# Optimization experiments

Hardware: AMD Instinct MI355X
Metric: run time of the kernel (lower is better)

Reference implementation:

```python
import jax, jax.numpy as jnp
import numpy as np

HEADS = 8
DIM = 512
DIM_HEAD = DIM // 8          # 64
LANDMARKS = DIM // 2         # 256
PINV_ITERS = 6
KERNEL = 33                  # residual_conv_kernel default
SCALE = DIM_HEAD ** -0.5


def setup_inputs() -> dict:
    key = jax.random.key(0)
    k0, k1, k2, k3 = jax.random.split(key, 4)
    b, n = 2, 8192
    x = jax.random.normal(k0, (b, n, DIM), dtype=jnp.float32)
    inner = HEADS * DIM_HEAD
    w_qkv = jax.random.normal(k1, (DIM, 3 * inner), dtype=jnp.float32) * 0.02
    w_out = jax.random.normal(k2, (inner, DIM), dtype=jnp.float32) * 0.02
    b_out = jnp.zeros((DIM,), dtype=jnp.float32)
    # grouped depthwise-over-heads conv: (out_ch=H, in_ch/groups=1, kH=33, kW=1)
    w_conv = jax.random.normal(k3, (HEADS, 1, KERNEL, 1), dtype=jnp.float32) * 0.02
    return {"x": x, "w_qkv": w_qkv, "w_out": w_out, "b_out": b_out, "w_conv": w_conv}


def _moore_penrose_pinv(x, iters=PINV_ITERS):
    # x: [b, h, m, m]
    abs_x = jnp.abs(x)
    col = abs_x.sum(axis=-1).max()   # global max over col sums (matches torch.max)
    row = abs_x.sum(axis=-2).max()
    z = jnp.swapaxes(x, -1, -2) / (col * row)
    I = jnp.eye(x.shape[-1], dtype=x.dtype)
    for _ in range(iters):
        xz = x @ z
        z = 0.25 * z @ (13.0 * I - xz @ (15.0 * I - xz @ (7.0 * I - xz)))
    return z


def reference(x, w_qkv, w_out, b_out, w_conv):
    b, n, _ = x.shape
    m = LANDMARKS
    l = n // m  # n chosen divisible by m, so no left-padding branch

    qkv = x @ w_qkv                                   # [b, n, 3*inner]
    q, k, v = jnp.split(qkv, 3, axis=-1)
    to_heads = lambda t: t.reshape(b, n, HEADS, DIM_HEAD).transpose(0, 2, 1, 3)
    q = to_heads(q) * SCALE                           # [b, h, n, d]
    k = to_heads(k)
    v = to_heads(v)

    # landmarks: mean over consecutive groups of l tokens -> [b, h, m, d]
    q_l = q.reshape(b, HEADS, m, l, DIM_HEAD).mean(axis=3)
    k_l = k.reshape(b, HEADS, m, l, DIM_HEAD).mean(axis=3)

    sim1 = jnp.einsum('bhid,bhjd->bhij', q, k_l)      # [b, h, n, m]
    sim2 = jnp.einsum('bhid,bhjd->bhij', q_l, k_l)    # [b, h, m, m]
    sim3 = jnp.einsum('bhid,bhjd->bhij', q_l, k)      # [b, h, m, n]

    attn1 = jax.nn.softmax(sim1, axis=-1)
    attn2 = jax.nn.softmax(sim2, axis=-1)
    attn3 = jax.nn.softmax(sim3, axis=-1)

    attn2_inv = _moore_penrose_pinv(attn2)
    out = attn1 @ (attn2_inv @ (attn3 @ v))           # [b, h, n, d]

    # residual depthwise conv over the sequence dim, per head (groups = heads)
    pad = KERNEL // 2
    res = jax.lax.conv_general_dilated(
        v, w_conv, window_strides=(1, 1), padding=((pad, pad), (0, 0)),
        dimension_numbers=('NCHW', 'OIHW', 'NCHW'), feature_group_count=HEADS)
    out = out + res

    out = out.transpose(0, 2, 1, 3).reshape(b, n, HEADS * DIM_HEAD)
    out = out @ w_out + b_out                         # to_out (dropout = eval no-op)
    return x + out                                    # NyAttenLayer residual
```

## Files before the change

### kernel.cpp

```cpp
#include <hip/hip_runtime.h>
#include <hip/hip_bf16.h>

#define BH 16
#define NTOK 8192
#define NHEAD 8
#define DH 64
#define MLM 256
#define QSCALE 0.125f
#define LP 72

typedef unsigned short ushort_t;
using frag_ab = __attribute__((ext_vector_type(8))) short;
using frag_cd = __attribute__((ext_vector_type(4))) float;

__device__ __forceinline__ unsigned short f2bs(float f){
  __hip_bfloat16 h = __float2bfloat16(f);
  return *(unsigned short*)&h;
}
__device__ __forceinline__ float bs2f(unsigned short u){
  union { unsigned int i; float f; } cv; cv.i = ((unsigned int)u) << 16; return cv.f;
}

__device__ __forceinline__ void gl_lds16(const unsigned short* g, unsigned short* l){
  __builtin_amdgcn_global_load_lds((const __attribute__((address_space(1))) unsigned int*)(const void*)g,
                                   (__attribute__((address_space(3))) unsigned int*)(void*)l, 16, 0, 0);
}

__global__ __launch_bounds__(256) void k_splitw(const float* __restrict__ in, int K, int N,
                                                unsigned short* __restrict__ oh,
                                                unsigned short* __restrict__ ol, int swz){
  const int idx = blockIdx.x * 256 + threadIdx.x;
  const int n = idx / K, k = idx - n * K;
  const float v = in[(size_t)k * N + n];
  const unsigned short hi = f2bs(v);
  int kd = k;
  if (swz){
    const int q = (k >> 3) & 3;
    kd = (k & ~31) | (((q ^ (n & 3)) & 3) << 3) | (k & 7);
  }
  oh[(size_t)n * K + kd] = hi;
  ol[(size_t)n * K + kd] = f2bs(v - bs2f(hi));
}

__global__ __launch_bounds__(256) void k_splitx(const float* __restrict__ in,
                                                unsigned short* __restrict__ oh,
                                                unsigned short* __restrict__ ol){
  const size_t i4 = ((size_t)blockIdx.x * 256 + threadIdx.x) * 4;
  const int row = (int)(i4 >> 9);
  const int col = (int)(i4 & 511);
  const int q = (col >> 3) & 3;
  const int cd = (col & ~31) | (((q ^ (row & 3)) & 3) << 3) | (col & 7);
  const size_t o4 = ((size_t)row << 9) + cd;
  float4 v = *(const float4*)(in + i4);
  const unsigned short h0 = f2bs(v.x), h1 = f2bs(v.y), h2 = f2bs(v.z), h3 = f2bs(v.w);
  *(ushort4*)(oh + o4) = make_ushort4(h0, h1, h2, h3);
  *(ushort4*)(ol + o4) = make_ushort4(f2bs(v.x - bs2f(h0)), f2bs(v.y - bs2f(h1)),
                                      f2bs(v.z - bs2f(h2)), f2bs(v.w - bs2f(h3)));
}

__global__ __launch_bounds__(256) void k_mfma_qkv(const unsigned short* __restrict__ xh,
                                                  const unsigned short* __restrict__ xl,
                                                  const unsigned short* __restrict__ bth,
                                                  const unsigned short* __restrict__ btl,
                                                  float* __restrict__ q,
                                                  unsigned short* __restrict__ kSh,
                                                  unsigned short* __restrict__ kSl,
                                                  float* __restrict__ v){
  const int n0 = blockIdx.x * 128;
  const int m0 = blockIdx.y * 128;
  __shared__ unsigned short Ah[128*32], Al[128*32], Bh[128*32], Bl[128*32];
  const int tid = threadIdx.x;
  const int wave = tid >> 6, lane = tid & 63;
  const int wm = wave >> 1, wn = wave & 1;
  const int lr = lane & 15, quad = lane >> 4;
  const int cswz = ((quad ^ (lr & 3)) & 3) << 3;
  const unsigned short* gsrc = (wave == 0) ? xh : (wave == 1) ? xl : (wave == 2) ? bth : btl;
  unsigned short* lbase = (wave == 0) ? Ah : (wave == 1) ? Al : (wave == 2) ? Bh : Bl;
  const int R0 = (wave < 2) ? m0 : n0;
  const int lrow = lane >> 2, lslot = (lane & 3) << 3;
  frag_cd acc[4][4];
#pragma unroll
  for (int mt = 0; mt < 4; mt++)
#pragma unroll
    for (int nt = 0; nt < 4; nt++){
      frag_cd z = {0.f, 0.f, 0.f, 0.f};
      acc[mt][nt] = z;
    }
  for (int k0 = 0; k0 < 512; k0 += 32){
    __syncthreads();
#pragma unroll
    for (int u = 0; u < 8; u++){
      gl_lds16(gsrc + (size_t)(R0 + u*16 + lrow) * 512 + k0 + lslot, lbase + u * 512);
    }
    __syncthreads();
    frag_ab a_h[4], a_l[4], b_h[4], b_l[4];
#pragma unroll
    for (int t = 0; t < 4; t++){
      const int ar = (wm*64 + t*16 + lr) << 5;
      const int br = (wn*64 + t*16 + lr) << 5;
      a_h[t] = *(const frag_ab*)&Ah[ar + cswz];
      a_l[t] = *(const frag_ab*)&Al[ar + cswz];
      b_h[t] = *(const frag_ab*)&Bh[br + cswz];
      b_l[t] = *(const frag_ab*)&Bl[br + cswz];
    }
#pragma unroll
    for (int mt = 0; mt < 4; mt++)
#pragma unroll
      for (int nt = 0; nt < 4; nt++){
        acc[mt][nt] = __builtin_amdgcn_mfma_f32_16x16x32_bf16(a_l[mt], b_h[nt], acc[mt][nt], 0, 0, 0);
        acc[mt][nt] = __builtin_amdgcn_mfma_f32_16x16x32_bf16(a_h[mt], b_l[nt], acc[mt][nt], 0, 0, 0);
        acc[mt][nt] = __builtin_amdgcn_mfma_f32_16x16x32_bf16(a_h[mt], b_h[nt], acc[mt][nt], 0, 0, 0);
      }
  }
#pragma unroll
  for (int mt = 0; mt < 4; mt++)
#pragma unroll
    for (int nt = 0; nt < 4; nt++)
#pragma unroll
      for (int rg = 0; rg < 4; rg++){
        const int row = m0 + wm*64 + mt*16 + quad*4 + rg;
        const int col = n0 + wn*64 + nt*16 + lr;
        const int bb = row >> 13, i = row & 8191;
        const int which = col >> 9;
        const int cc = col & 511;
        const int h = cc >> 6, d = cc & 63;
        const size_t off = (((size_t)(bb * NHEAD + h)) * NTOK + i) * DH + d;
        const float val = acc[mt][nt][rg];
        if (which == 0)      q[off] = val * QSCALE;
        else if (which == 1){
          const unsigned short hi = f2bs(val);
          kSh[off] = hi; kSl[off] = f2bs(val - bs2f(hi));
        }
        else                 v[off] = val;
      }
}

__global__ __launch_bounds__(256) void k_mfma_final(const unsigned int* __restrict__ qpk,
                                                    const unsigned short* __restrict__ bth,
                                                    const unsigned short* __restrict__ btl,
                                                    const float* __restrict__ xin,
                                                    const float* __restrict__ bout,
                                                    float* __restrict__ outp){
  const int n0 = blockIdx.x * 128;
  const int m0 = blockIdx.y * 128;
  __shared__ unsigned short Ah[128][40], Al[128][40], Bh[128][40], Bl[128][40];
  const int tid = threadIdx.x;
  const int wave = tid >> 6, lane = tid & 63;
  const int wm = wave >> 1, wn = wave & 1;
  const int lr = lane & 15, quad = lane >> 4, koff = quad * 8;
  const int bb = m0 >> 13;
  frag_cd acc[4][4];
#pragma unroll
  for (int mt = 0; mt < 4; mt++)
#pragma unroll
    for (int nt = 0; nt < 4; nt++){
      frag_cd z = {0.f, 0.f, 0.f, 0.f};
      acc[mt][nt] = z;
    }
  for (int k0 = 0; k0 < 512; k0 += 32){
    const int h = k0 >> 6, dbase = k0 & 63;
    __syncthreads();
#pragma unroll
    for (int u = 0; u < 4; u++){
      const int f = tid + u * 256, row = f >> 3, c4 = (f & 7) << 2;
      const int i = (m0 + row) & 8191;
      uint4 pw = *(const uint4*)(qpk + (((size_t)(bb * NHEAD + h)) * NTOK + i) * DH + dbase + c4);
      *(ushort4*)&Ah[row][c4] = make_ushort4((unsigned short)pw.x, (unsigned short)pw.y,
                                             (unsigned short)pw.z, (unsigned short)pw.w);
      *(ushort4*)&Al[row][c4] = make_ushort4((unsigned short)(pw.x >> 16), (unsigned short)(pw.y >> 16),
                                             (unsigned short)(pw.z >> 16), (unsigned short)(pw.w >> 16));
    }
#pragma unroll
    for (int u = 0; u < 2; u++){
      const int f = tid + u * 256, row = f >> 2, ch = (f & 3) << 3;
      *(uint4*)&Bh[row][ch] = *(const uint4*)(bth + (size_t)(n0 + row) * 512 + k0 + ch);
      *(uint4*)&Bl[row][ch] = *(const uint4*)(btl + (size_t)(n0 + row) * 512 + k0 + ch);
    }
    __syncthreads();
    frag_ab a_h[4], a_l[4], b_h[4], b_l[4];
#pragma unroll
    for (int t = 0; t < 4; t++){
      a_h[t] = *(const frag_ab*)&Ah[wm*64 + t*16 + lr][koff];
      a_l[t] = *(const frag_ab*)&Al[wm*64 + t*16 + lr][koff];
      b_h[t] = *(const frag_ab*)&Bh[wn*64 + t*16 + lr][koff];
      b_l[t] = *(const frag_ab*)&Bl[wn*64 + t*16 + lr][koff];
    }
#pragma unroll
    for (int mt = 0; mt < 4; mt++)
#pragma unroll
      for (int nt = 0; nt < 4; nt++){
        acc[mt][nt] = __builtin_amdgcn_mfma_f32_16x16x32_bf16(a_l[mt], b_h[nt], acc[mt][nt], 0, 0, 0);
        acc[mt][nt] = __builtin_amdgcn_mfma_f32_16x16x32_bf16(a_h[mt], b_l[nt], acc[mt][nt], 0, 0, 0);
        acc[mt][nt] = __builtin_amdgcn_mfma_f32_16x16x32_bf16(a_h[mt], b_h[nt], acc[mt][nt], 0, 0, 0);
      }
  }
#pragma unroll
  for (int mt = 0; mt < 4; mt++)
#pragma unroll
    for (int nt = 0; nt < 4; nt++)
#pragma unroll
      for (int rg = 0; rg < 4; rg++){
        const int row = m0 + wm*64 + mt*16 + quad*4 + rg;
        const int col = n0 + wn*64 + nt*16 + lr;
        outp[(size_t)row * 512 + col] = acc[mt][nt][rg] + bout[col] + xin[(size_t)row * 512 + col];
      }
}

__global__ __launch_bounds__(64) void k_land2(const float* __restrict__ qf,
                                              const unsigned short* __restrict__ kSh,
                                              const unsigned short* __restrict__ kSl,
                                              float* __restrict__ qlf, float* __restrict__ klf,
                                              unsigned short* __restrict__ qlSh, unsigned short* __restrict__ qlSl,
                                              unsigned short* __restrict__ klSh, unsigned short* __restrict__ klSl){
  const int isK = blockIdx.y;
  float* dst = isK ? klf : qlf;
  unsigned short* dh = isK ? klSh : qlSh;
  unsigned short* dl = isK ? klSl : qlSl;
  const int bh = blockIdx.x >> 8;
  const int j  = blockIdx.x & 255;
  const int d  = threadIdx.x;
  const size_t base = ((size_t)bh * NTOK + (size_t)j * 32) * DH + d;
  float s = 0.f;
  if (!isK){
    const float* p = qf + base;
#pragma unroll
    for (int t = 0; t < 32; t++) s += p[t * DH];
  } else {
    const unsigned short* ph = kSh + base;
    const unsigned short* pl = kSl + base;
#pragma unroll
    for (int t = 0; t < 32; t++) s += bs2f(ph[t * DH]) + bs2f(pl[t * DH]);
  }
  const float val = s * (1.f / 32.f);
  const size_t oidx = ((size_t)bh * MLM + j) * DH + d;
  dst[oidx] = val;
  const unsigned short hi = f2bs(val);
  dh[oidx] = hi;
  dl[oidx] = f2bs(val - bs2f(hi));
}

__global__ __launch_bounds__(256) void k_vtrans(const float* __restrict__ vf,
                                                unsigned short* __restrict__ vTh,
                                                unsigned short* __restrict__ vTl){
  __shared__ float T[64][68];
  const int j0 = blockIdx.x * 64, bh = blockIdx.y;
  const int tid = threadIdx.x;
#pragma unroll
  for (int u = 0; u < 4; u++){
    const int f = tid + u * 256, row = f >> 4, c4 = (f & 15) << 2;
    *(float4*)&T[row][c4] = *(const float4*)(vf + ((size_t)bh * NTOK + j0 + row) * DH + c4);
  }
  __syncthreads();
#pragma unroll
  for (int u = 0; u < 4; u++){
    const int f = tid + u * 256, d = f >> 4, j4 = (f & 15) << 2;
    const float v0 = T[j4+0][d], v1 = T[j4+1][d], v2 = T[j4+2][d], v3 = T[j4+3][d];
    const unsigned short h0 = f2bs(v0), h1 = f2bs(v1), h2 = f2bs(v2), h3 = f2bs(v3);
    const size_t off = ((size_t)bh * DH + d) * NTOK + j0 + j4;
    *(ushort4*)(vTh + off) = make_ushort4(h0, h1, h2, h3);
    *(ushort4*)(vTl + off) = make_ushort4(f2bs(v0 - bs2f(h0)), f2bs(v1 - bs2f(h1)),
                                          f2bs(v2 - bs2f(h2)), f2bs(v3 - bs2f(h3)));
  }
}

__global__ __launch_bounds__(256) void k_sim2(const float* __restrict__ qlf,
                                              const float* __restrict__ klf,
                                              float* __restrict__ C){
  const int bh = blockIdx.z;
  const float* Ab = qlf + (size_t)bh * MLM * DH;
  const float* Bb = klf + (size_t)bh * MLM * DH;
  float* Cb = C + (size_t)bh * MLM * MLM;
  const int n0 = blockIdx.x * 64;
  const int m0 = blockIdx.y * 64;
  __shared__ float As[16][64];
  __shared__ float Bs[16][64];
  const int tid = threadIdx.x, ty = tid >> 4, tx = tid & 15;
  const int lm = tid >> 2, lk = (tid & 3) << 2;
  float acc[4][4] = {};
  for (int k0 = 0; k0 < 64; k0 += 16){
    float4 a4 = *(const float4*)(Ab + (size_t)(m0 + lm) * DH + k0 + lk);
    As[lk+0][lm] = a4.x; As[lk+1][lm] = a4.y; As[lk+2][lm] = a4.z; As[lk+3][lm] = a4.w;
    float4 b4 = *(const float4*)(Bb + (size_t)(n0 + lm) * DH + k0 + lk);
    Bs[lk+0][lm] = b4.x; Bs[lk+1][lm] = b4.y; Bs[lk+2][lm] = b4.z; Bs[lk+3][lm] = b4.w;
    __syncthreads();
#pragma unroll
    for (int kk = 0; kk < 16; kk++){
      float a[4], bv[4];
#pragma unroll
      for (int r = 0; r < 4; r++) a[r] = As[kk][ty*4 + r];
#pragma unroll
      for (int c = 0; c < 4; c++) bv[c] = Bs[kk][tx*4 + c];
#pragma unroll
      for (int r = 0; r < 4; r++)
#pragma unroll
        for (int c = 0; c < 4; c++) acc[r][c] += a[r] * bv[c];
    }
    __syncthreads();
  }
#pragma unroll
  for (int r = 0; r < 4; r++)
#pragma unroll
    for (int c = 0; c < 4; c++)
      Cb[(size_t)(m0 + ty*4 + r) * MLM + n0 + tx*4 + c] = acc[r][c];
}

__global__ __launch_bounds__(256) void k_softmax256(const float* __restrict__ in, float* __restrict__ outp){
  const int row = blockIdx.x;
  const int t = threadIdx.x;
  float v = in[(size_t)row * 256 + t];
  __shared__ float red[256];
  red[t] = v; __syncthreads();
  for (int o = 128; o > 0; o >>= 1){ if (t < o) red[t] = fmaxf(red[t], red[t+o]); __syncthreads(); }
  float mx = red[0]; __syncthreads();
  float e = expf(v - mx);
  red[t] = e; __syncthreads();
  for (int o = 128; o > 0; o >>= 1){ if (t < o) red[t] += red[t+o]; __syncthreads(); }
  outp[(size_t)row * 256 + t] = e / red[0];
}

__global__ __launch_bounds__(256) void k_colrow(const float* __restrict__ a2, float* __restrict__ part){
  const int bh = blockIdx.x;
  const int t = threadIdx.x;
  const float* p = a2 + (size_t)bh * 65536;
  float cs = 0.f;
  for (int i = 0; i < 256; i++) cs += fabsf(p[(size_t)i * 256 + t]);
  __shared__ float r2[256];
  r2[t] = cs; __syncthreads();
  for (int o = 128; o > 0; o >>= 1){
    if (t < o) r2[t] = fmaxf(r2[t], r2[t+o]);
    __syncthreads();
  }
  if (t == 0) part[bh] = r2[0];
}

__global__ __launch_bounds__(256) void k_z0(const float* __restrict__ a2, const float* __restrict__ part,
                                            float* __restrict__ z,
                                            unsigned short* __restrict__ zTh,
                                            unsigned short* __restrict__ zTl){
  const int bh = blockIdx.x >> 8;
  const int i  = blockIdx.x & 255;
  const int j  = threadIdx.x;
  float m2 = 0.f;
#pragma unroll
  for (int t = 0; t < 16; t++) m2 = fmaxf(m2, part[t]);
  const float sc = 1.f / m2;
  const size_t ridx = ((size_t)bh * 256 + j) * 256 + i;
  const float val = a2[ridx] * sc;
  z[((size_t)bh * 256 + i) * 256 + j] = val;
  const unsigned short hi = f2bs(val);
  zTh[ridx] = hi;
  zTl[ridx] = f2bs(val - bs2f(hi));
}

__global__ __launch_bounds__(256) void k_gemm256m(const float* __restrict__ A,
                                                  const unsigned short* __restrict__ BTh,
                                                  const unsigned short* __restrict__ BTl,
                                                  const float* __restrict__ D,
                                                  float* __restrict__ C,
                                                  unsigned short* __restrict__ CTh,
                                                  unsigned short* __restrict__ CTl,
                                                  float c0, float s0, int wC){
  __shared__ unsigned short Ah[32][40], Al[32][40], Bh[64][40], Bl[64][40];
  __shared__ float Ct[64][33];
  const int bh = blockIdx.y, tile = blockIdx.x;
  const int m0 = (tile >> 2) * 32, n0 = (tile & 3) * 64;
  const size_t bo = (size_t)bh * 65536;
  const int tid = threadIdx.x;
  const int wave = tid >> 6, lane = tid & 63;
  const int wm = wave >> 1, wn = wave & 1;
  const int lr = lane & 15, quad = lane >> 4, koff = quad * 8;
  const int ar = tid >> 3, ac = (tid & 7) << 2;
  const int br = tid >> 2, bc = (tid & 3) << 3;
  frag_cd acc[2];
  { frag_cd z = {0.f,0.f,0.f,0.f}; acc[0] = z; acc[1] = z; }
  float4 ra  = *(const float4*)(A + bo + (size_t)(m0 + ar) * 256 + ac);
  uint4  rbh = *(const uint4*)(BTh + bo + (size_t)(n0 + br) * 256 + bc);
  uint4  rbl = *(const uint4*)(BTl + bo + (size_t)(n0 + br) * 256 + bc);
  for (int k0 = 0; k0 < 256; k0 += 32){
    __syncthreads();
    {
      const unsigned short h0=f2bs(ra.x),h1=f2bs(ra.y),h2=f2bs(ra.z),h3=f2bs(ra.w);
      *(ushort4*)&Ah[ar][ac] = make_ushort4(h0,h1,h2,h3);
      *(ushort4*)&Al[ar][ac] = make_ushort4(f2bs(ra.x-bs2f(h0)), f2bs(ra.y-bs2f(h1)),
                                            f2bs(ra.z-bs2f(h2)), f2bs(ra.w-bs2f(h3)));
      *(uint4*)&Bh[br][bc] = rbh;
      *(uint4*)&Bl[br][bc] = rbl;
    }
    __syncthreads();
    if (k0 < 224){
      ra  = *(const float4*)(A + bo + (size_t)(m0 + ar) * 256 + k0 + 32 + ac);
      rbh = *(const uint4*)(BTh + bo + (size_t)(n0 + br) * 256 + k0 + 32 + bc);
      rbl = *(const uint4*)(BTl + bo + (size_t)(n0 + br) * 256 + k0 + 32 + bc);
    }
    frag_ab a_h = *(const frag_ab*)&Ah[wm*16 + lr][koff];
    frag_ab a_l = *(const frag_ab*)&Al[wm*16 + lr][koff];
#pragma unroll
    for (int b = 0; b < 2; b++){
      frag_ab b_h = *(const frag_ab*)&Bh[wn*32 + b*16 + lr][koff];
      frag_ab b_l = *(const frag_ab*)&Bl[wn*32 + b*16 + lr][koff];
      acc[b] = __builtin_amdgcn_mfma_f32_16x16x32_bf16(a_l, b_l, acc[b], 0, 0, 0);
      acc[b] = __builtin_amdgcn_mfma_f32_16x16x32_bf16(a_l, b_h, acc[b], 0, 0, 0);
      acc[b] = __builtin_amdgcn_mfma_f32_16x16x32_bf16(a_h, b_l, acc[b], 0, 0, 0);
      acc[b] = __builtin_amdgcn_mfma_f32_16x16x32_bf16(a_h, b_h, acc[b], 0, 0, 0);
    }
  }
  const bool useD = (c0 != 0.f);
#pragma unroll
  for (int b = 0; b < 2; b++)
#pragma unroll
    for (int rg = 0; rg < 4; rg++){
      const int row = m0 + wm*16 + quad*4 + rg;
      const int col = n0 + wn*32 + b*16 + lr;
      const size_t idx = bo + (size_t)row * 256 + col;
      const float dv = useD ? D[idx] : 0.f;
      const float val = s0 * (c0 * dv - acc[b][rg]);
      if (wC) C[idx] = val;
      Ct[col - n0][row - m0] = val;
    }
  __syncthreads();
  {
    const int cr = tid >> 2, sg = (tid & 3) << 3;
    unsigned int ph[4], pl[4];
#pragma unroll
    for (int j = 0; j < 4; j++){
      const float v0 = Ct[cr][sg + 2*j], v1 = Ct[cr][sg + 2*j + 1];
      const unsigned short h0 = f2bs(v0), h1 = f2bs(v1);
      ph[j] = (unsigned int)h0 | ((unsigned int)h1 << 16);
      pl[j] = (unsigned int)f2bs(v0 - bs2f(h0)) | ((unsigned int)f2bs(v1 - bs2f(h1)) << 16);
    }
    const size_t tb = bo + (size_t)(n0 + cr) * 256 + m0 + sg;
    *(uint4*)(CTh + tb) = make_uint4(ph[0], ph[1], ph[2], ph[3]);
    *(uint4*)(CTl + tb) = make_uint4(pl[0], pl[1], pl[2], pl[3]);
  }
}

__global__ __launch_bounds__(256) void k_flash(const unsigned short* __restrict__ qlSh,
                                               const unsigned short* __restrict__ qlSl,
                                               const unsigned short* __restrict__ kSh,
                                               const unsigned short* __restrict__ kSl,
                                               const unsigned short* __restrict__ vTh,
                                               const unsigned short* __restrict__ vTl,
                                               float* __restrict__ pbuf){
  extern __shared__ __align__(16) unsigned short sm[];
  unsigned short* Kh  = sm;
  unsigned short* Kl  = sm + 1*64*LP;
  unsigned short* Wth = sm + 2*64*LP;
  unsigned short* Wtl = sm + 3*64*LP;
  const int kc = blockIdx.x, mt = blockIdx.y, bh = blockIdx.z;
  const int m0 = mt * 64, kbeg = kc * 512;
  const int tid = threadIdx.x;
  const int wave = tid >> 6, lane = tid & 63;
  const int lr = lane & 15, quad = lane >> 4;
  const size_t qbase = (size_t)bh * MLM * DH;
  const size_t kb  = (size_t)bh * NTOK * DH;
  const size_t vtb = (size_t)bh * DH * NTOK;
#pragma unroll
  for (int u = 0; u < 4; u++){
    const int f = tid + u * 256, row = f >> 4, c4 = (f & 15) << 2;
    *(ushort4*)&Kh[row*LP + c4] = *(const ushort4*)(qlSh + qbase + (size_t)(m0 + row) * DH + c4);
    *(ushort4*)&Kl[row*LP + c4] = *(const ushort4*)(qlSl + qbase + (size_t)(m0 + row) * DH + c4);
  }
  __syncthreads();
  frag_ab qa_h[2], qa_l[2];
#pragma unroll
  for (int ks = 0; ks < 2; ks++){
    const int ao = (wave*16 + lr)*LP + ks*32 + quad*8;
    qa_h[ks] = *(const frag_ab*)&Kh[ao];
    qa_l[ks] = *(const frag_ab*)&Kl[ao];
  }
  float m_run[4], l_run[4];
  frag_cd o[4];
#pragma unroll
  for (int r = 0; r < 4; r++){ m_run[r] = -1e30f; l_run[r] = 0.f; }
#pragma unroll
  for (int nt = 0; nt < 4; nt++){ frag_cd z = {0.f,0.f,0.f,0.f}; o[nt] = z; }

  for (int ch = 0; ch < 8; ch++){
    const int kr0 = kbeg + ch * 64;
    __syncthreads();
#pragma unroll
    for (int u = 0; u < 4; u++){
      const int f = tid + u * 256, row = f >> 4, c4 = (f & 15) << 2;
      *(ushort4*)&Kh[row*LP + c4]  = *(const ushort4*)(kSh + kb + (size_t)(kr0 + row) * DH + c4);
      *(ushort4*)&Kl[row*LP + c4]  = *(const ushort4*)(kSl + kb + (size_t)(kr0 + row) * DH + c4);
      *(ushort4*)&Wth[row*LP + c4] = *(const ushort4*)(vTh + vtb + (size_t)row * NTOK + kr0 + c4);
      *(ushort4*)&Wtl[row*LP + c4] = *(const ushort4*)(vTl + vtb + (size_t)row * NTOK + kr0 + c4);
    }
    __syncthreads();
    frag_cd s[4];
#pragma unroll
    for (int nt = 0; nt < 4; nt++){ frag_cd z = {0.f,0.f,0.f,0.f}; s[nt] = z; }
#pragma unroll
    for (int ks = 0; ks < 2; ks++){
#pragma unroll
      for (int nt = 0; nt < 4; nt++){
        const int bo = (nt*16 + lr)*LP + ks*32 + quad*8;
        frag_ab b_h = *(const frag_ab*)&Kh[bo];
        frag_ab b_l = *(const frag_ab*)&Kl[bo];
        s[nt] = __builtin_amdgcn_mfma_f32_16x16x32_bf16(qa_l[ks], b_h, s[nt], 0, 0, 0);
        s[nt] = __builtin_amdgcn_mfma_f32_16x16x32_bf16(qa_h[ks], b_l, s[nt], 0, 0, 0);
        s[nt] = __builtin_amdgcn_mfma_f32_16x16x32_bf16(qa_h[ks], b_h, s[nt], 0, 0, 0);
      }
    }
    __syncthreads();
#pragma unroll
    for (int rg = 0; rg < 4; rg++){
      float mx = fmaxf(fmaxf(s[0][rg], s[1][rg]), fmaxf(s[2][rg], s[3][rg]));
#pragma unroll
      for (int o2 = 8; o2 >= 1; o2 >>= 1) mx = fmaxf(mx, __shfl_xor(mx, o2));
      const float mnew = fmaxf(m_run[rg], mx);
      float e0 = expf(s[0][rg] - mnew), e1 = expf(s[1][rg] - mnew);
      float e2 = expf(s[2][rg] - mnew), e3 = expf(s[3][rg] - mnew);
      float psum = e0 + e1 + e2 + e3;
#pragma unroll
      for (int o2 = 8; o2 >= 1; o2 >>= 1) psum += __shfl_xor(psum, o2);
      const float alpha = expf(m_run[rg] - mnew);
      l_run[rg] = l_run[rg] * alpha + psum;
      m_run[rg] = mnew;
#pragma unroll
      for (int nt = 0; nt < 4; nt++) o[nt][rg] *= alpha;
      const int prow = (wave*16 + quad*4 + rg) * LP;
      float ee[4] = {e0, e1, e2, e3};
#pragma unroll
      for (int nt = 0; nt < 4; nt++){
        const unsigned short hh = f2bs(ee[nt]);
        Kh[prow + nt*16 + lr] = hh;
        Kl[prow + nt*16 + lr] = f2bs(ee[nt] - bs2f(hh));
      }
    }
#pragma unroll
    for (int ks = 0; ks < 2; ks++){
      const int ao = (wave*16 + lr)*LP + ks*32 + quad*8;
      frag_ab p_h = *(const frag_ab*)&Kh[ao];
      frag_ab p_l = *(const frag_ab*)&Kl[ao];
#pragma unroll
      for (int nt = 0; nt < 4; nt++){
        const int bo = (nt*16 + lr)*LP + ks*32 + quad*8;
        frag_ab b_h = *(const frag_ab*)&Wth[bo];
        frag_ab b_l = *(const frag_ab*)&Wtl[bo];
        o[nt] = __builtin_amdgcn_mfma_f32_16x16x32_bf16(p_l, b_h, o[nt], 0, 0, 0);
        o[nt] = __builtin_amdgcn_mfma_f32_16x16x32_bf16(p_h, b_l, o[nt], 0, 0, 0);
        o[nt] = __builtin_amdgcn_mfma_f32_16x16x32_bf16(p_h, b_h, o[nt], 0, 0, 0);
      }
    }
  }
  float* pb = pbuf + (((size_t)bh * 16 + kc) * 256 + m0) * 68;
#pragma unroll
  for (int rg = 0; rg < 4; rg++){
    const int row = wave*16 + quad*4 + rg;
#pragma unroll
    for (int nt = 0; nt < 4; nt++)
      pb[(size_t)row * 68 + nt*16 + lr] = o[nt][rg];
    if (lr == 0){
      pb[(size_t)row * 68 + 64] = m_run[rg];
      pb[(size_t)row * 68 + 65] = l_run[rg];
    }
  }
}

__global__ __launch_bounds__(256) void k_comb(const float* __restrict__ pbuf, float* __restrict__ av){
  const int wv = threadIdx.x >> 6, lane = threadIdx.x & 63;
  const int id = blockIdx.x * 4 + wv;
  const int bh = id >> 8, row = id & 255;
  const float* base = pbuf + ((size_t)bh * 16 * 256 + row) * 68;
  float M = -1e30f;
#pragma unroll
  for (int k = 0; k < 16; k++) M = fmaxf(M, base[(size_t)k * 256 * 68 + 64]);
  float L = 0.f, o = 0.f;
#pragma unroll
  for (int k = 0; k < 16; k++){
    const float* p = base + (size_t)k * 256 * 68;
    float w = expf(p[64] - M);
    L += p[65] * w;
    o += p[lane] * w;
  }
  av[((size_t)bh * MLM + row) * DH + lane] = o / L;
}

__global__ __launch_bounds__(256) void k_w2(const float* __restrict__ Z, const float* __restrict__ AV,
                                            float* __restrict__ W2,
                                            unsigned short* __restrict__ w2Th,
                                            unsigned short* __restrict__ w2Tl){
  const int bh = blockIdx.y, mt = blockIdx.x;
  const float* Zb = Z + (size_t)bh * 65536;
  const float* Vb = AV + (size_t)bh * MLM * DH;
  float* Wb = W2 + (size_t)bh * MLM * DH;
  const int m0 = mt * 64;
  __shared__ float As[16][64];
  __shared__ float Bs[16][64];
  const int tid = threadIdx.x, ty = tid >> 4, tx = tid & 15;
  const int lm = tid >> 2, lk = (tid & 3) << 2;
  const int lk2 = tid >> 4, ln = (tid & 15) << 2;
  float acc[4][4] = {};
  for (int k0 = 0; k0 < 256; k0 += 16){
    float4 a4 = *(const float4*)(Zb + (size_t)(m0 + lm) * 256 + k0 + lk);
    As[lk+0][lm] = a4.x; As[lk+1][lm] = a4.y; As[lk+2][lm] = a4.z; As[lk+3][lm] = a4.w;
    float4 b4 = *(const float4*)(Vb + (size_t)(k0 + lk2) * DH + ln);
    *(float4*)&Bs[lk2][ln] = b4;
    __syncthreads();
#pragma unroll
    for (int kk = 0; kk < 16; kk++){
      float a[4], bv[4];
#pragma unroll
      for (int r = 0; r < 4; r++) a[r] = As[kk][ty*4 + r];
#pragma unroll
      for (int c = 0; c < 4; c++) bv[c] = Bs[kk][tx*4 + c];
#pragma unroll
      for (int r = 0; r < 4; r++)
#pragma unroll
        for (int c = 0; c < 4; c++) acc[r][c] += a[r] * bv[c];
    }
    __syncthreads();
  }
#pragma unroll
  for (int r = 0; r < 4; r++)
#pragma unroll
    for (int c = 0; c < 4; c++){
      const float val = acc[r][c];
      Wb[(size_t)(m0 + ty*4 + r) * DH + tx*4 + c] = val;
      const unsigned short hi = f2bs(val);
      const size_t tidx = ((size_t)bh * DH + tx*4 + c) * MLM + m0 + ty*4 + r;
      w2Th[tidx] = hi;
      w2Tl[tidx] = f2bs(val - bs2f(hi));
    }
}

__global__ __launch_bounds__(256) void k_attn1(float* __restrict__ qoh,
                                               const unsigned short* __restrict__ klSh,
                                               const unsigned short* __restrict__ klSl,
                                               const float* __restrict__ vf,
                                               const unsigned short* __restrict__ w2Th,
                                               const unsigned short* __restrict__ w2Tl,
                                               const float* __restrict__ wconv){
  extern __shared__ __align__(16) unsigned short sm[];
  unsigned short* Kh  = sm;
  unsigned short* Kl  = sm + 1*64*LP;
  unsigned short* Wth = sm + 2*64*LP;
  unsigned short* Wtl = sm + 3*64*LP;
  float (*Vs)[68] = (float (*)[68])sm;
  float (*St)[68] = (float (*)[68])sm;
  __shared__ float wcs[33];
  const int it = blockIdx.x, bh = blockIdx.y, h = bh & 7;
  const int i0 = it * 64;
  float* qb = qoh + (size_t)bh * NTOK * DH;
  const int tid = threadIdx.x;
  const int wave = tid >> 6, lane = tid & 63;
  const int lr = lane & 15, quad = lane >> 4;
  if (tid < 33) wcs[tid] = wconv[h*33 + tid];
#pragma unroll
  for (int u = 0; u < 4; u++){
    const int f = tid + u * 256, row = f >> 4, c4 = (f & 15) << 2;
    float4 a4 = *(const float4*)(qb + (size_t)(i0 + row) * DH + c4);
    const unsigned short h0 = f2bs(a4.x), h1 = f2bs(a4.y), h2 = f2bs(a4.z), h3 = f2bs(a4.w);
    *(ushort4*)&Kh[row*LP + c4] = make_ushort4(h0, h1, h2, h3);
    *(ushort4*)&Kl[row*LP + c4] = make_ushort4(f2bs(a4.x - bs2f(h0)), f2bs(a4.y - bs2f(h1)),
                                               f2bs(a4.z - bs2f(h2)), f2bs(a4.w - bs2f(h3)));
  }
  __syncthreads();
  frag_ab qa_h[2], qa_l[2];
#pragma unroll
  for (int ks = 0; ks < 2; ks++){
    const int ao = (wave*16 + lr)*LP + ks*32 + quad*8;
    qa_h[ks] = *(const frag_ab*)&Kh[ao];
    qa_l[ks] = *(const frag_ab*)&Kl[ao];
  }
  float m_run[4], l_run[4];
  frag_cd o[4];
#pragma unroll
  for (int r = 0; r < 4; r++){ m_run[r] = -1e30f; l_run[r] = 0.f; }
#pragma unroll
  for (int nt = 0; nt < 4; nt++){ frag_cd z = {0.f,0.f,0.f,0.f}; o[nt] = z; }
  const size_t klbase = (size_t)bh * MLM * DH;
  const size_t wtbase = (size_t)bh * DH * MLM;

  for (int jc = 0; jc < 4; jc++){
    const int j0 = jc * 64;
    __syncthreads();
#pragma unroll
    for (int u = 0; u < 4; u++){
      const int f = tid + u * 256, row = f >> 4, c4 = (f & 15) << 2;
      *(ushort4*)&Kh[row*LP + c4]  = *(const ushort4*)(klSh + klbase + (size_t)(j0 + row) * DH + c4);
      *(ushort4*)&Kl[row*LP + c4]  = *(const ushort4*)(klSl + klbase + (size_t)(j0 + row) * DH + c4);
      *(ushort4*)&Wth[row*LP + c4] = *(const ushort4*)(w2Th + wtbase + (size_t)row * MLM + j0 + c4);
      *(ushort4*)&Wtl[row*LP + c4] = *(const ushort4*)(w2Tl + wtbase + (size_t)row * MLM + j0 + c4);
    }
    __syncthreads();
    frag_cd s[4];
#pragma unroll
    for (int nt = 0; nt < 4; nt++){ frag_cd z = {0.f,0.f,0.f,0.f}; s[nt] = z; }
#pragma unroll
    for (int ks = 0; ks < 2; ks++){
#pragma unroll
      for (int nt = 0; nt < 4; nt++){
        const int bo = (nt*16 + lr)*LP + ks*32 + quad*8;
        frag_ab b_h = *(const frag_ab*)&Kh[bo];
        frag_ab b_l = *(const frag_ab*)&Kl[bo];
        s[nt] = __builtin_amdgcn_mfma_f32_16x16x32_bf16(qa_l[ks], b_h, s[nt], 0, 0, 0);
        s[nt] = __builtin_amdgcn_mfma_f32_16x16x32_bf16(qa_h[ks], b_l, s[nt], 0, 0, 0);
        s[nt] = __builtin_amdgcn_mfma_f32_16x16x32_bf16(qa_h[ks], b_h, s[nt], 0, 0, 0);
      }
    }
    __syncthreads();
#pragma unroll
    for (int rg = 0; rg < 4; rg++){
      float mx = fmaxf(fmaxf(s[0][rg], s[1][rg]), fmaxf(s[2][rg], s[3][rg]));
#pragma unroll
      for (int o2 = 8; o2 >= 1; o2 >>= 1) mx = fmaxf(mx, __shfl_xor(mx, o2));
      const float mnew = fmaxf(m_run[rg], mx);
      float e0 = expf(s[0][rg] - mnew), e1 = expf(s[1][rg] - mnew);
      float e2 = expf(s[2][rg] - mnew), e3 = expf(s[3][rg] - mnew);
      float psum = e0 + e1 + e2 + e3;
#pragma unroll
      for (int o2 = 8; o2 >= 1; o2 >>= 1) psum += __shfl_xor(psum, o2);
      const float alpha = expf(m_run[rg] - mnew);
      l_run[rg] = l_run[rg] * alpha + psum;
      m_run[rg] = mnew;
#pragma unroll
      for (int nt = 0; nt < 4; nt++) o[nt][rg] *= alpha;
      const int prow = (wave*16 + quad*4 + rg) * LP;
      float ee[4] = {e0, e1, e2, e3};
#pragma unroll
      for (int nt = 0; nt < 4; nt++){
        const unsigned short hh = f2bs(ee[nt]);
        Kh[prow + nt*16 + lr] = hh;
        Kl[prow + nt*16 + lr] = f2bs(ee[nt] - bs2f(hh));
      }
    }
#pragma unroll
    for (int ks = 0; ks < 2; ks++){
      const int ao = (wave*16 + lr)*LP + ks*32 + quad*8;
      frag_ab p_h = *(const frag_ab*)&Kh[ao];
      frag_ab p_l = *(const frag_ab*)&Kl[ao];
#pragma unroll
      for (int nt = 0; nt < 4; nt++){
        const int bo = (nt*16 + lr)*LP + ks*32 + quad*8;
        frag_ab b_h = *(const frag_ab*)&Wth[bo];
        frag_ab b_l = *(const frag_ab*)&Wtl[bo];
        o[nt] = __builtin_amdgcn_mfma_f32_16x16x32_bf16(p_l, b_h, o[nt], 0, 0, 0);
        o[nt] = __builtin_amdgcn_mfma_f32_16x16x32_bf16(p_h, b_l, o[nt], 0, 0, 0);
        o[nt] = __builtin_amdgcn_mfma_f32_16x16x32_bf16(p_h, b_h, o[nt], 0, 0, 0);
      }
    }
  }
#pragma unroll
  for (int rg = 0; rg < 4; rg++){
    const float inv = 1.f / l_run[rg];
#pragma unroll
    for (int nt = 0; nt < 4; nt++) o[nt][rg] *= inv;
  }
  __syncthreads();
#pragma unroll
  for (int u = 0; u < 6; u++){
    const int f = tid + u * 256, row = f >> 4, c4 = (f & 15) << 2;
    const int g = i0 - 16 + row;
    float4 vv = make_float4(0.f, 0.f, 0.f, 0.f);
    if (g >= 0 && g < NTOK) vv = *(const float4*)(vf + ((size_t)bh * NTOK + g) * DH + c4);
    *(float4*)&Vs[row][c4] = vv;
  }
  __syncthreads();
  const int rbase = wave*16 + quad*4;
#pragma unroll
  for (int nt = 0; nt < 4; nt++){
    const int col = nt*16 + lr;
#pragma unroll
    for (int s5 = 0; s5 < 36; s5++){
      const float v = Vs[rbase + s5][col];
#pragma unroll
      for (int rg = 0; rg < 4; rg++){
        const int t = s5 - rg;
        if (t >= 0 && t <= 32) o[nt][rg] += wcs[t] * v;
      }
    }
  }
  __syncthreads();
#pragma unroll
  for (int nt = 0; nt < 4; nt++)
#pragma unroll
    for (int rg = 0; rg < 4; rg++){
      const float val = o[nt][rg];
      const unsigned short hi = f2bs(val);
      const unsigned short lo = f2bs(val - bs2f(hi));
      St[rbase + rg][nt*16 + lr] = __uint_as_float((unsigned int)hi | ((unsigned int)lo << 16));
    }
  __syncthreads();
#pragma unroll
  for (int u = 0; u < 4; u++){
    const int f = tid + u * 256, row = f >> 4, c4 = (f & 15) << 2;
    *(float4*)(qb + (size_t)(i0 + row) * DH + c4) = *(const float4*)&St[row][c4];
  }
}

extern "C" void kernel_launch(void* const* d_in, const int* in_sizes, int n_in,
                              void* d_out, int out_size, void* d_ws, size_t ws_size,
                              hipStream_t stream){
  (void)in_sizes; (void)n_in; (void)out_size; (void)ws_size;
  const float* x     = (const float*)d_in[0];
  const float* wqkv  = (const float*)d_in[1];
  const float* wout  = (const float*)d_in[2];
  const float* bout  = (const float*)d_in[3];
  const float* wconv = (const float*)d_in[4];
  float* outp = (float*)d_out;

  char* base = (char*)d_ws;
  auto alloc = [&](size_t bytes)->char*{
    char* p = base; base += (bytes + 255) & ~(size_t)255; return p;
  };
  const size_t QS = (size_t)BH * NTOK * DH;
  const size_t LS = (size_t)BH * MLM * DH;
  const size_t MM = (size_t)BH * MLM * MLM;

  float* qf   = (float*)alloc(QS * 4);
  float* vf   = (float*)alloc(QS * 4);
  unsigned short* kSh = (unsigned short*)alloc(QS * 2);
  unsigned short* kSl = (unsigned short*)alloc(QS * 2);
  float* qlf  = (float*)alloc(LS * 4);
  float* klf  = (float*)alloc(LS * 4);
  float* a2   = (float*)alloc(MM * 4);
  float* zb   = (float*)alloc(MM * 4);
  float* z2   = (float*)alloc(MM * 4);
  float* xz   = (float*)alloc(MM * 4);
  float* t2   = (float*)alloc(MM * 4);
  float* t4   = (float*)alloc(MM * 4);
  float* part = (float*)alloc(64 * 4);
  char* un = alloc(10 * MM * 2);
  unsigned short* pl0 = (unsigned short*)un;
  unsigned short* zbTh = pl0 + 0*MM; unsigned short* zbTl = pl0 + 1*MM;
  unsigned short* z2Th = pl0 + 2*MM; unsigned short* z2Tl = pl0 + 3*MM;
  unsigned short* xzTh = pl0 + 4*MM; unsigned short* xzTl = pl0 + 5*MM;
  unsigned short* t2Th = pl0 + 6*MM; unsigned short* t2Tl = pl0 + 7*MM;
  unsigned short* t4Th = pl0 + 8*MM; unsigned short* t4Tl = pl0 + 9*MM;
  float* pbuf = (float*)un;
  float* av   = (float*)alloc(LS * 4);
  float* w2   = (float*)alloc(LS * 4);
  unsigned short* wqTh = (unsigned short*)alloc((size_t)1536 * 512 * 2);
  unsigned short* wqTl = (unsigned short*)alloc((size_t)1536 * 512 * 2);
  unsigned short* woTh = (unsigned short*)alloc((size_t)512 * 512 * 2);
  unsigned short* woTl = (unsigned short*)alloc((size_t)512 * 512 * 2);
  unsigned short* qlSh = (unsigned short*)alloc(LS * 2);
  unsigned short* qlSl = (unsigned short*)alloc(LS * 2);
  unsigned short* klSh = (unsigned short*)alloc(LS * 2);
  unsigned short* klSl = (unsigned short*)alloc(LS * 2);
  unsigned short* w2Th = (unsigned short*)alloc(LS * 2);
  unsigned short* w2Tl = (unsigned short*)alloc(LS * 2);
  unsigned short* vTh  = (unsigned short*)alloc(QS * 2);
  unsigned short* vTl  = (unsigned short*)alloc(QS * 2);
  unsigned short* xh = vTh;
  unsigned short* xl = vTl;

  k_splitw<<<1536 * 512 / 256, 256, 0, stream>>>(wqkv, 512, 1536, wqTh, wqTl, 1);
  k_splitw<<<512 * 512 / 256, 256, 0, stream>>>(wout, 512, 512, woTh, woTl, 0);
  k_splitx<<<8192, 256, 0, stream>>>(x, xh, xl);
  k_mfma_qkv<<<dim3(12, 128), 256, 0, stream>>>(xh, xl, wqTh, wqTl, qf, kSh, kSl, vf);
  k_vtrans<<<dim3(NTOK / 64, BH), 256, 0, stream>>>(vf, vTh, vTl);
  k_land2<<<dim3(BH * MLM, 2), 64, 0, stream>>>(qf, kSh, kSl, qlf, klf, qlSh, qlSl, klSh, klSl);
  k_sim2<<<dim3(4, 4, BH), 256, 0, stream>>>(qlf, klf, xz);
  k_softmax256<<<BH * MLM, 256, 0, stream>>>(xz, a2);
  k_colrow<<<BH, 256, 0, stream>>>(a2, part);
  k_z0<<<BH * MLM, 256, 0, stream>>>(a2, part, zb, zbTh, zbTl);
  {
    float* zc = zb;  unsigned short* zcTh = zbTh; unsigned short* zcTl = zbTl;
    float* zn = z2;  unsigned short* znTh = z2Th; unsigned short* znTl = z2Tl;
    for (int it = 0; it < 6; ++it){
      k_gemm256m<<<dim3(32, BH), 256, 0, stream>>>(a2, zcTh, zcTl, a2, xz, xzTh, xzTl, 0.f, -1.f, 1);
      k_gemm256m<<<dim3(32, BH), 256, 0, stream>>>(xz, xzTh, xzTl, xz, t2, t2Th, t2Tl, 7.f, 1.f, 0);
      k_gemm256m<<<dim3(32, BH), 256, 0, stream>>>(xz, t2Th, t2Tl, xz, t4, t4Th, t4Tl, 15.f, 1.f, 0);
      k_gemm256m<<<dim3(32, BH), 256, 0, stream>>>(zc, t4Th, t4Tl, zc, zn, znTh, znTl, 13.f, 0.25f, 1);
      float* tf = zc; zc = zn; zn = tf;
      unsigned short* th = zcTh; zcTh = znTh; znTh = th;
      unsigned short* tl = zcTl; zcTl = znTl; znTl = tl;
    }
  }
  const size_t FLASH_LDS = (size_t)4 * 64 * LP * 2;
  k_flash<<<dim3(16, 4, BH), 256, FLASH_LDS, stream>>>(qlSh, qlSl, kSh, kSl, vTh, vTl, pbuf);
  k_comb<<<BH * MLM / 4, 256, 0, stream>>>(pbuf, av);
  k_w2<<<dim3(4, BH), 256, 0, stream>>>(zb, av, w2, w2Th, w2Tl);
  k_attn1<<<dim3(128, BH), 256, FLASH_LDS, stream>>>(qf, klSh, klSl, vf, w2Th, w2Tl, wconv);
  k_mfma_final<<<dim3(4, 128), 256, 0, stream>>>((const unsigned int*)qf, woTh, woTl, x, bout, outp);
}
```

Baseline: 715.7 us.

## Enlarge attn1 tiles to 128 rows, give P its own LDS, load Q directly

k_attn1 now runs 512 threads over 128 query rows per block. Each 64-row K/W2 landmark chunk staged in LDS is therefore shared by twice as many queries, and the grid is halved. The softmax probabilities get separate LDS buffers (Ph/Pl), which removes one barrier per chunk, and Q fragments are loaded and split into hi/lo bf16 straight from global memory instead of going through LDS. expf is also replaced with exp2f of a pre-scaled argument in several softmax kernels. The cost is double the LDS per block and fewer blocks, which can lower occupancy.

```diff
diff --git a/kernel.cpp b/kernel.cpp
--- a/kernel.cpp
+++ b/kernel.cpp
@@ -8,6 +8,7 @@
 #define MLM 256
 #define QSCALE 0.125f
 #define LP 72
+#define LOG2E 1.4426950408889634f
 
 typedef unsigned short ushort_t;
 using frag_ab = __attribute__((ext_vector_type(8))) short;
@@ -312,7 +313,7 @@
   red[t] = v; __syncthreads();
   for (int o = 128; o > 0; o >>= 1){ if (t < o) red[t] = fmaxf(red[t], red[t+o]); __syncthreads(); }
   float mx = red[0]; __syncthreads();
-  float e = expf(v - mx);
+  float e = exp2f((v - mx) * LOG2E);
   red[t] = e; __syncthreads();
   for (int o = 128; o > 0; o >>= 1){ if (t < o) red[t] += red[t+o]; __syncthreads(); }
   outp[(size_t)row * 256 + t] = e / red[0];
@@ -509,12 +510,12 @@
 #pragma unroll
       for (int o2 = 8; o2 >= 1; o2 >>= 1) mx = fmaxf(mx, __shfl_xor(mx, o2));
       const float mnew = fmaxf(m_run[rg], mx);
-      float e0 = expf(s[0][rg] - mnew), e1 = expf(s[1][rg] - mnew);
-      float e2 = expf(s[2][rg] - mnew), e3 = expf(s[3][rg] - mnew);
+      float e0 = exp2f((s[0][rg] - mnew) * LOG2E), e1 = exp2f((s[1][rg] - mnew) * LOG2E);
+      float e2 = exp2f((s[2][rg] - mnew) * LOG2E), e3 = exp2f((s[3][rg] - mnew) * LOG2E);
       float psum = e0 + e1 + e2 + e3;
 #pragma unroll
       for (int o2 = 8; o2 >= 1; o2 >>= 1) psum += __shfl_xor(psum, o2);
-      const float alpha = expf(m_run[rg] - mnew);
+      const float alpha = exp2f((m_run[rg] - mnew) * LOG2E);
       l_run[rg] = l_run[rg] * alpha + psum;
       m_run[rg] = mnew;
 #pragma unroll
@@ -570,7 +571,7 @@
 #pragma unroll
   for (int k = 0; k < 16; k++){
     const float* p = base + (size_t)k * 256 * 68;
-    float w = expf(p[64] - M);
+    float w = exp2f((p[64] - M) * LOG2E);
     L += p[65] * w;
     o += p[lane] * w;
   }
@@ -625,7 +626,7 @@
     }
 }
 
-__global__ __launch_bounds__(256) void k_attn1(float* __restrict__ qoh,
+__global__ __launch_bounds__(512) void k_attn1(float* __restrict__ qoh,
                                                const unsigned short* __restrict__ klSh,
                                                const unsigned short* __restrict__ klSl,
                                                const float* __restrict__ vf,
@@ -637,32 +638,33 @@
   unsigned short* Kl  = sm + 1*64*LP;
   unsigned short* Wth = sm + 2*64*LP;
   unsigned short* Wtl = sm + 3*64*LP;
+  unsigned short* Ph  = sm + 4*64*LP;
+  unsigned short* Pl  = sm + 6*64*LP;
   float (*Vs)[68] = (float (*)[68])sm;
   float (*St)[68] = (float (*)[68])sm;
   __shared__ float wcs[33];
   const int it = blockIdx.x, bh = blockIdx.y, h = bh & 7;
-  const int i0 = it * 64;
+  const int i0 = it * 128;
   float* qb = qoh + (size_t)bh * NTOK * DH;
   const int tid = threadIdx.x;
   const int wave = tid >> 6, lane = tid & 63;
   const int lr = lane & 15, quad = lane >> 4;
   if (tid < 33) wcs[tid] = wconv[h*33 + tid];
-#pragma unroll
-  for (int u = 0; u < 4; u++){
-    const int f = tid + u * 256, row = f >> 4, c4 = (f & 15) << 2;
-    float4 a4 = *(const float4*)(qb + (size_t)(i0 + row) * DH + c4);
-    const unsigned short h0 = f2bs(a4.x), h1 = f2bs(a4.y), h2 = f2bs(a4.z), h3 = f2bs(a4.w);
-    *(ushort4*)&Kh[row*LP + c4] = make_ushort4(h0, h1, h2, h3);
-    *(ushort4*)&Kl[row*LP + c4] = make_ushort4(f2bs(a4.x - bs2f(h0)), f2bs(a4.y - bs2f(h1)),
-                                               f2bs(a4.z - bs2f(h2)), f2bs(a4.w - bs2f(h3)));
-  }
-  __syncthreads();
   frag_ab qa_h[2], qa_l[2];
 #pragma unroll
   for (int ks = 0; ks < 2; ks++){
-    const int ao = (wave*16 + lr)*LP + ks*32 + quad*8;
-    qa_h[ks] = *(const frag_ab*)&Kh[ao];
-    qa_l[ks] = *(const frag_ab*)&Kl[ao];
+    const float* qsrc = qb + (size_t)(i0 + wave*16 + lr) * DH + ks*32 + quad*8;
+    float4 a0 = *(const float4*)qsrc;
+    float4 a1 = *(const float4*)(qsrc + 4);
+    float vv[8] = {a0.x, a0.y, a0.z, a0.w, a1.x, a1.y, a1.z, a1.w};
+    frag_ab fh, fl;
+#pragma unroll
+    for (int j = 0; j < 8; j++){
+      const unsigned short hb = f2bs(vv[j]);
+      fh[j] = (short)hb;
+      fl[j] = (short)f2bs(vv[j] - bs2f(hb));
+    }
+    qa_h[ks] = fh; qa_l[ks] = fl;
   }
   float m_run[4], l_run[4];
   frag_cd o[4];
@@ -677,8 +679,8 @@
     const int j0 = jc * 64;
     __syncthreads();
 #pragma unroll
-    for (int u = 0; u < 4; u++){
-      const int f = tid + u * 256, row = f >> 4, c4 = (f & 15) << 2;
+    for (int u = 0; u < 2; u++){
+      const int f = tid + u * 512, row = f >> 4, c4 = (f & 15) << 2;
       *(ushort4*)&Kh[row*LP + c4]  = *(const ushort4*)(klSh + klbase + (size_t)(j0 + row) * DH + c4);
       *(ushort4*)&Kl[row*LP + c4]  = *(const ushort4*)(klSl + klbase + (size_t)(j0 + row) * DH + c4);
       *(ushort4*)&Wth[row*LP + c4] = *(const ushort4*)(w2Th + wtbase + (size_t)row * MLM + j0 + c4);
@@ -700,19 +702,18 @@
         s[nt] = __builtin_amdgcn_mfma_f32_16x16x32_bf16(qa_h[ks], b_h, s[nt], 0, 0, 0);
       }
     }
-    __syncthreads();
 #pragma unroll
     for (int rg = 0; rg < 4; rg++){
       float mx = fmaxf(fmaxf(s[0][rg], s[1][rg]), fmaxf(s[2][rg], s[3][rg]));
 #pragma unroll
       for (int o2 = 8; o2 >= 1; o2 >>= 1) mx = fmaxf(mx, __shfl_xor(mx, o2));
       const float mnew = fmaxf(m_run[rg], mx);
-      float e0 = expf(s[0][rg] - mnew), e1 = expf(s[1][rg] - mnew);
-      float e2 = expf(s[2][rg] - mnew), e3 = expf(s[3][rg] - mnew);
+      float e0 = exp2f((s[0][rg] - mnew) * LOG2E), e1 = exp2f((s[1][rg] - mnew) * LOG2E);
+      float e2 = exp2f((s[2][rg] - mnew) * LOG2E), e3 = exp2f((s[3][rg] - mnew) * LOG2E);
       float psum = e0 + e1 + e2 + e3;
 #pragma unroll
       for (int o2 = 8; o2 >= 1; o2 >>= 1) psum += __shfl_xor(psum, o2);
-      const float alpha = expf(m_run[rg] - mnew);
+      const float alpha = exp2f((m_run[rg] - mnew) * LOG2E);
       l_run[rg] = l_run[rg] * alpha + psum;
       m_run[rg] = mnew;
 #pragma unroll
@@ -722,15 +723,15 @@
 #pragma unroll
       for (int nt = 0; nt < 4; nt++){
         const unsigned short hh = f2bs(ee[nt]);
-        Kh[prow + nt*16 + lr] = hh;
-        Kl[prow + nt*16 + lr] = f2bs(ee[nt] - bs2f(hh));
+        Ph[prow + nt*16 + lr] = hh;
+        Pl[prow + nt*16 + lr] = f2bs(ee[nt] - bs2f(hh));
       }
     }
 #pragma unroll
     for (int ks = 0; ks < 2; ks++){
       const int ao = (wave*16 + lr)*LP + ks*32 + quad*8;
-      frag_ab p_h = *(const frag_ab*)&Kh[ao];
-      frag_ab p_l = *(const frag_ab*)&Kl[ao];
+      frag_ab p_h = *(const frag_ab*)&Ph[ao];
+      frag_ab p_l = *(const frag_ab*)&Pl[ao];
 #pragma unroll
       for (int nt = 0; nt < 4; nt++){
         const int bo = (nt*16 + lr)*LP + ks*32 + quad*8;
@@ -750,8 +751,8 @@
   }
   __syncthreads();
 #pragma unroll
-  for (int u = 0; u < 6; u++){
-    const int f = tid + u * 256, row = f >> 4, c4 = (f & 15) << 2;
+  for (int u = 0; u < 5; u++){
+    const int f = tid + u * 512, row = f >> 4, c4 = (f & 15) << 2;
     const int g = i0 - 16 + row;
     float4 vv = make_float4(0.f, 0.f, 0.f, 0.f);
     if (g >= 0 && g < NTOK) vv = *(const float4*)(vf + ((size_t)bh * NTOK + g) * DH + c4);
@@ -785,7 +786,7 @@
   __syncthreads();
 #pragma unroll
   for (int u = 0; u < 4; u++){
-    const int f = tid + u * 256, row = f >> 4, c4 = (f & 15) << 2;
+    const int f = tid + u * 512, row = f >> 4, c4 = (f & 15) << 2;
     *(float4*)(qb + (size_t)(i0 + row) * DH + c4) = *(const float4*)&St[row][c4];
   }
 }
@@ -871,9 +872,10 @@
     }
   }
   const size_t FLASH_LDS = (size_t)4 * 64 * LP * 2;
+  const size_t ATTN1_LDS = (size_t)8 * 64 * LP * 2;
   k_flash<<<dim3(16, 4, BH), 256, FLASH_LDS, stream>>>(qlSh, qlSl, kSh, kSl, vTh, vTl, pbuf);
   k_comb<<<BH * MLM / 4, 256, 0, stream>>>(pbuf, av);
   k_w2<<<dim3(4, BH), 256, 0, stream>>>(zb, av, w2, w2Th, w2Tl);
-  k_attn1<<<dim3(128, BH), 256, FLASH_LDS, stream>>>(qf, klSh, klSl, vf, w2Th, w2Tl, wconv);
+  k_attn1<<<dim3(64, BH), 512, ATTN1_LDS, stream>>>(qf, klSh, klSl, vf, w2Th, w2Tl, wconv);
   k_mfma_final<<<dim3(4, 128), 256, 0, stream>>>((const unsigned int*)qf, woTh, woTl, x, bout, outp);
 }
```

Result: faster. 695.9 us (-2.8%).
